# Performance work log

Measured on AMD Instinct MI355X. Metric: run time of the kernel, lower is better.

## Reference

```python
import jax, jax.numpy as jnp
import numpy as np

SIMPLE_W = 1.0
NON_SIMPLE_W = 5.0

# connectivity offset sets (exclude center)
_ALL26 = [(a, b, c) for a in (-1, 0, 1) for b in (-1, 0, 1) for c in (-1, 0, 1) if (a, b, c) != (0, 0, 0)]
OFF6 = [o for o in _ALL26 if abs(o[0]) + abs(o[1]) + abs(o[2]) == 1]          # scipy default structure
OFF18 = [o for o in _ALL26 if not (abs(o[0]) == 1 and abs(o[1]) == 1 and abs(o[2]) == 1)]  # the 's' structure
OFF26 = _ALL26                                                                  # np.ones((3,3,3))


def global_label(fg):
    """Connected-component labels (6-connectivity) via max-propagation.
    Labels are distinct positive ints per component (values differ from scipy's
    1..K but only label *equality* is used downstream). fg: bool [D,H,W]."""
    D, H, W = fg.shape
    idx = (jnp.arange(fg.size, dtype=jnp.int32) + 1).reshape(fg.shape)
    lab0 = jnp.where(fg, idx, 0)

    def step(lab):
        p = jnp.pad(lab, 1)
        m = lab
        for dz, dy, dx in OFF6:
            m = jnp.maximum(m, p[1 + dz:1 + dz + D, 1 + dy:1 + dy + H, 1 + dx:1 + dx + W])
        return jnp.where(fg, m, 0)

    def cond(c):
        return ~c[1]

    def body(c):
        lab, _ = c
        new = step(lab)
        return new, jnp.all(new == lab)

    lab, _ = jax.lax.while_loop(cond, body, (lab0, jnp.array(False)))
    return lab


def local_ncomp(mask, offsets):
    """Number of connected components inside each 3x3x3 window.
    mask: bool [N,3,3,3]. Max-propagation of unique seeds for 26 iters
    (>= max path length among 27 voxels); a component is counted where the
    surviving max label equals its own seed."""
    seed = (jnp.arange(27, dtype=jnp.int32) + 1).reshape(3, 3, 3)
    lab0 = jnp.where(mask, seed, 0)

    def body(_, lab):
        p = jnp.pad(lab, ((0, 0), (1, 1), (1, 1), (1, 1)))
        m = lab
        for dz, dy, dx in offsets:
            m = jnp.maximum(m, p[:, 1 + dz:4 + dz, 1 + dy:4 + dy, 1 + dx:4 + dx])
        return jnp.where(mask, m, 0)

    lab = jax.lax.fori_loop(0, 26, body, lab0)
    return jnp.sum((lab == seed) & mask, axis=(1, 2, 3))


def nonsimple_map(x):
    """Per-voxel non-simple-point indicator, float, same shape as x."""
    D, H, W = x.shape
    fg = x > 0
    glab = global_label(fg)
    p = jnp.pad(glab, 1, mode='edge')  # np.pad(..., 'edge')
    # 3x3x3 label windows per voxel -> [N,3,3,3]
    wins = jnp.stack([p[dz:dz + D, dy:dy + H, dx:dx + W]
                      for dz in range(3) for dy in range(3) for dx in range(3)], axis=-1)
    wins = wins.reshape(-1, 3, 3, 3)
    center = wins[:, 1, 1, 1]  # [N]
    c = center[:, None, None, None]
    # test 1: complement-of-center-label components (18-connectivity) must be exactly 1
    n1 = local_ncomp(wins != c, OFF18)
    # test 2: center-label components with center voxel removed (26-conn) must be exactly 1
    mask2 = (wins == c).at[:, 1, 1, 1].set(False)
    n2 = local_ncomp(mask2, OFF26)
    ns = (center != 0) & ((n1 != 1) | (n2 != 1))
    return ns.reshape(D, H, W).astype(x.dtype)


def setup_inputs() -> dict:
    key = jax.random.key(0)
    k1, k2 = jax.random.split(key)
    D = H = W = 64
    prediction = jax.random.normal(k1, (D, H, W), dtype=jnp.float32)
    label = jax.random.randint(k2, (D, H, W), 0, 2).astype(jnp.float32)
    return {"prediction": prediction, "label": label}


def reference(prediction, label):
    pw = nonsimple_map(prediction)
    lw = nonsimple_map(label)
    w_bool = (pw + lw) > 0
    weight = jnp.where(w_bool, NON_SIMPLE_W, SIMPLE_W).astype(prediction.dtype)
    # BCEWithLogitsLoss(reduction='none'): max(x,0) - x*y + log(1+exp(-|x|))
    cost = jnp.maximum(prediction, 0.0) - prediction * label + jnp.log1p(jnp.exp(-jnp.abs(prediction)))
    return jnp.mean(weight * cost)
```

## Files before the change

### kernel.cpp

```cpp
#include <hip/hip_runtime.h>

#define DIM 64
#define NVOX (DIM * DIM * DIM)
#define EPF 53248

__device__ __forceinline__ int find_root_link(int* L, int v) {
    for (;;) {
        int p = L[v];
        if (p == v) return v;
        int gp = L[p];
        if (gp == p) return p;
        L[v] = gp;
        v = gp;
    }
}

__device__ __forceinline__ void unite(int* L, int a, int b) {
    int ra = find_root_link(L, a);
    int rb = find_root_link(L, b);
    while (ra != rb) {
        if (ra > rb) { int t = ra; ra = rb; rb = t; }
        int old = atomicCAS(&L[rb], rb, ra);
        if (old == rb) break;
        rb = find_root_link(L, old);
        ra = find_root_link(L, ra);
    }
}

__device__ __forceinline__ int chase(const int* __restrict__ L, int p) {
    int q = L[p];
    while (q != p) { p = q; q = L[p]; }
    return p;
}

__global__ void local_ccl(const float* __restrict__ pred,
                          const float* __restrict__ lab,
                          int* __restrict__ LP, int* __restrict__ LL,
                          float* __restrict__ out) {
    __shared__ int s_lab[2048];
    int t = threadIdx.x;
    if (blockIdx.x == 0 && blockIdx.y == 0 && t == 0) *out = 0.0f;
    int b = blockIdx.x;
    int tx = b & 3, ty = (b >> 2) & 3, tz = b >> 4;
    int X0 = tx << 4, Y0 = ty << 4, Z0 = tz << 3;

    const float* src = blockIdx.y ? lab : pred;
    int* Lg = blockIdx.y ? LL : LP;

    bool fg[8];
    int vv[8];
#pragma unroll
    for (int i = 0; i < 8; ++i) {
        int l = t + (i << 8);
        int v = ((Z0 + (l >> 8)) << 12) | ((Y0 + ((l >> 4) & 15)) << 6)
              | (X0 + (l & 15));
        vv[i] = v;
        fg[i] = src[v] > 0.0f;
        s_lab[l] = fg[i] ? l : -1;
    }
    __syncthreads();

#pragma unroll
    for (int i = 0; i < 8; ++i) {
        if (!fg[i]) continue;
        int l = t + (i << 8);
        int lx = l & 15, ly = (l >> 4) & 15, lz = l >> 8;
        if (lx < 15 && s_lab[l + 1]   >= 0) unite(s_lab, l, l + 1);
        if (ly < 15 && s_lab[l + 16]  >= 0) unite(s_lab, l, l + 16);
        if (lz < 7  && s_lab[l + 256] >= 0) unite(s_lab, l, l + 256);
    }
    __syncthreads();

#pragma unroll
    for (int i = 0; i < 8; ++i) {
        int g = -1;
        if (fg[i]) {
            int p = s_lab[t + (i << 8)];
            while (s_lab[p] != p) p = s_lab[p];
            g = ((Z0 + (p >> 8)) << 12) | ((Y0 + ((p >> 4) & 15)) << 6)
              | (X0 + (p & 15));
        }
        Lg[vv[i]] = g;
    }
}

__global__ void boundary_link(int* __restrict__ LP, int* __restrict__ LL) {
    int r = blockIdx.x * blockDim.x + threadIdx.x;
    int v, n;
    if (r < 12288) {
        int plane = 15 + ((r >> 12) << 4);
        int ij = r & 4095;
        v = ((ij >> 6) << 12) | ((ij & 63) << 6) | plane;
        n = v + 1;
    } else if (r < 24576) {
        int r2 = r - 12288;
        int plane = 15 + ((r2 >> 12) << 4);
        int ij = r2 & 4095;
        v = ((ij >> 6) << 12) | (plane << 6) | (ij & 63);
        n = v + 64;
    } else {
        int r3 = r - 24576;
        int plane = 7 + ((r3 >> 12) << 3);
        int ij = r3 & 4095;
        v = (plane << 12) | ((ij >> 6) << 6) | (ij & 63);
        n = v + 4096;
    }

    int pa = LP[v], pb = LP[n];
    int la = LL[v], lb = LL[n];
    bool doP = (pa >= 0) & (pb >= 0);
    bool doL = (la >= 0) & (lb >= 0);

    int rp0 = -1, rp1 = -1, rl0 = -1, rl1 = -1;
    if (doP) {
        int x0 = chase(LP, pa), x1 = chase(LP, pb);
        rp0 = min(x0, x1); rp1 = max(x0, x1);
    }
    if (doL) {
        int x0 = chase(LL, la), x1 = chase(LL, lb);
        rl0 = min(x0, x1); rl1 = max(x0, x1);
    }

    int lane = threadIdx.x & 63;
    int qp0 = __shfl_up(rp0, 1, 64), qp1 = __shfl_up(rp1, 1, 64);
    int ql0 = __shfl_up(rl0, 1, 64), ql1 = __shfl_up(rl1, 1, 64);
    bool dupP = lane && (qp0 == rp0) && (qp1 == rp1);
    bool dupL = lane && (ql0 == rl0) && (ql1 == rl1);

    if (doP && !dupP && rp0 != rp1) unite(LP, rp0, rp1);
    if (doL && !dupL && rl0 != rl1) unite(LL, rl0, rl1);
}

#define MX_L 0x6DB6DB6u
#define MX_R 0x36DB6DBu
#define MY_L 0x7E3F1F8u
#define MY_R 0x0FC7E3Fu
#define M27  0x7FFFFFFu

__device__ __forceinline__ unsigned dil26(unsigned m) {
    m |= ((m << 1) & MX_L) | ((m >> 1) & MX_R);
    m |= ((m << 3) & MY_L) | ((m >> 3) & MY_R);
    m |= ((m << 9) & M27)  | (m >> 9);
    return m;
}
__device__ __forceinline__ unsigned dil18(unsigned m) {
    unsigned ax = m | ((m << 1) & MX_L) | ((m >> 1) & MX_R);
    unsigned ay = m | ((m << 3) & MY_L) | ((m >> 3) & MY_R);
    unsigned dxy = ax | ((ax << 3) & MY_L) | ((ax >> 3) & MY_R);
    unsigned dxz = ax | ((ax << 9) & M27)  | (ax >> 9);
    unsigned dyz = ay | ((ay << 9) & M27)  | (ay >> 9);
    return dxy | dxz | dyz;
}

__device__ __forceinline__ bool single18(unsigned m) {
    if (!m) return false;
    unsigned c = m & (~m + 1u);
    for (;;) {
        unsigned n = dil18(c) & m;
        if (n == m) return true;
        if (n == c) return false;
        c = n;
    }
}
__device__ __forceinline__ bool single26(unsigned m) {
    if (!m) return false;
    unsigned c = m & (~m + 1u);
    for (;;) {
        unsigned n = dil26(c) & m;
        if (n == m) return true;
        if (n == c) return false;
        c = n;
    }
}

#define HV 600

__global__ void finalize_kernel(const float* __restrict__ pred,
                                const float* __restrict__ lab,
                                const int* __restrict__ LP,
                                const int* __restrict__ LL,
                                float* __restrict__ out) {
    __shared__ int sP[HV], sL[HV];
    __shared__ float s_part[4];
    int t = threadIdx.x;
    int b = blockIdx.x;
    int tx = b & 7, ty = (b >> 3) & 7, tz = b >> 6;
    int x0 = tx << 3, y0 = ty << 3, z0 = tz << 2;

    for (int i = t; i < HV; i += 256) {
        int hx = i % 10, r = i / 10, hy = r % 10, hz = r / 10;
        int gx = x0 + hx - 1; gx = gx < 0 ? 0 : (gx > 63 ? 63 : gx);
        int gy = y0 + hy - 1; gy = gy < 0 ? 0 : (gy > 63 ? 63 : gy);
        int gz = z0 + hz - 1; gz = gz < 0 ? 0 : (gz > 63 ? 63 : gz);
        int gv = (gz << 12) | (gy << 6) | gx;
        int p = LP[gv];
        if (p >= 0) p = chase(LP, p);
        sP[i] = p;
        p = LL[gv];
        if (p >= 0) p = chase(LL, p);
        sL[i] = p;
    }
    __syncthreads();

    int lx = t & 7, ly = (t >> 3) & 7, lz = t >> 6;
    int x = x0 | lx, y = y0 | ly, z = z0 | lz;
    int v = (z << 12) | (y << 6) | x;
    int base = lz * 100 + ly * 10 + lx;

    bool nsP = false, nsL = false;
    {
        int c = sP[base + 111];
        if (c >= 0) {
            unsigned m1 = 0, m2 = 0; int k = 0;
#pragma unroll
            for (int kz = 0; kz < 3; ++kz)
#pragma unroll
                for (int ky = 0; ky < 3; ++ky)
#pragma unroll
                    for (int kx = 0; kx < 3; ++kx, ++k) {
                        int w = sP[base + kz * 100 + ky * 10 + kx];
                        m1 |= (unsigned)(w != c) << k;
                        m2 |= (unsigned)(w == c) << k;
                    }
            m2 &= ~(1u << 13);
            nsP = !(single18(m1) && single26(m2));
        }
    }
    {
        int c = sL[base + 111];
        if (c >= 0) {
            unsigned m1 = 0, m2 = 0; int k = 0;
#pragma unroll
            for (int kz = 0; kz < 3; ++kz)
#pragma unroll
                for (int ky = 0; ky < 3; ++ky)
#pragma unroll
                    for (int kx = 0; kx < 3; ++kx, ++k) {
                        int w = sL[base + kz * 100 + ky * 10 + kx];
                        m1 |= (unsigned)(w != c) << k;
                        m2 |= (unsigned)(w == c) << k;
                    }
            m2 &= ~(1u << 13);
            nsL = !(single18(m1) && single26(m2));
        }
    }

    float p = pred[v], l = lab[v];
    float cost = fmaxf(p, 0.0f) - p * l + log1pf(__expf(-fabsf(p)));
    float w = (nsP || nsL) ? 5.0f : 1.0f;
    float contrib = w * cost;

#pragma unroll
    for (int off = 32; off > 0; off >>= 1)
        contrib += __shfl_down(contrib, off, 64);
    if ((t & 63) == 0) s_part[t >> 6] = contrib;
    __syncthreads();
    if (t == 0) {
        float s = s_part[0] + s_part[1] + s_part[2] + s_part[3];
        atomicAdd(out, s * (1.0f / (float)NVOX));
    }
}

extern "C" void kernel_launch(void* const* d_in, const int* in_sizes, int n_in,
                              void* d_out, int out_size, void* d_ws, size_t ws_size,
                              hipStream_t stream) {
    const float* pred = (const float*)d_in[0];
    const float* lab  = (const float*)d_in[1];
    float* out = (float*)d_out;

    int* LP = (int*)d_ws;
    int* LL = LP + NVOX;

    hipLaunchKernelGGL(local_ccl, dim3(128, 2), dim3(256), 0, stream,
                       pred, lab, LP, LL, out);
    hipLaunchKernelGGL(boundary_link, dim3(EPF / 256), dim3(256), 0, stream,
                       LP, LL);
    hipLaunchKernelGGL(finalize_kernel, dim3(NVOX / 256), dim3(256), 0, stream,
                       pred, lab, LP, LL, out);
}
```

Baseline: 114.1 us.

## Enlarge finalize tiles to 8x8x8, batch halo loads, skip duplicate boundary chases

```diff
diff --git a/kernel.cpp b/kernel.cpp
--- a/kernel.cpp
+++ b/kernel.cpp
@@ -106,29 +106,35 @@
         n = v + 4096;
     }
 
+    int lane = threadIdx.x & 63;
+
     int pa = LP[v], pb = LP[n];
     int la = LL[v], lb = LL[n];
     bool doP = (pa >= 0) & (pb >= 0);
     bool doL = (la >= 0) & (lb >= 0);
 
+    int xpa = __shfl_up(pa, 1, 64), xpb = __shfl_up(pb, 1, 64);
+    int xla = __shfl_up(la, 1, 64), xlb = __shfl_up(lb, 1, 64);
+    if (lane && xpa == pa && xpb == pb) doP = false;
+    if (lane && xla == la && xlb == lb) doL = false;
+
     int rp0 = -1, rp1 = -1, rl0 = -1, rl1 = -1;
     if (doP) {
-        int x0 = chase(LP, pa), x1 = chase(LP, pb);
-        rp0 = min(x0, x1); rp1 = max(x0, x1);
+        int u0 = chase(LP, pa), u1 = chase(LP, pb);
+        rp0 = min(u0, u1); rp1 = max(u0, u1);
     }
     if (doL) {
-        int x0 = chase(LL, la), x1 = chase(LL, lb);
-        rl0 = min(x0, x1); rl1 = max(x0, x1);
-    }
-
-    int lane = threadIdx.x & 63;
+        int u0 = chase(LL, la), u1 = chase(LL, lb);
+        rl0 = min(u0, u1); rl1 = max(u0, u1);
+    }
+
     int qp0 = __shfl_up(rp0, 1, 64), qp1 = __shfl_up(rp1, 1, 64);
     int ql0 = __shfl_up(rl0, 1, 64), ql1 = __shfl_up(rl1, 1, 64);
     bool dupP = lane && (qp0 == rp0) && (qp1 == rp1);
     bool dupL = lane && (ql0 == rl0) && (ql1 == rl1);
 
-    if (doP && !dupP && rp0 != rp1) unite(LP, rp0, rp1);
-    if (doL && !dupL && rl0 != rl1) unite(LL, rl0, rl1);
+    if (rp0 >= 0 && rp0 != rp1 && !dupP) unite(LP, rp0, rp1);
+    if (rl0 >= 0 && rl0 != rl1 && !dupL) unite(LL, rl0, rl1);
 }
 
 #define MX_L 0x6DB6DB6u
@@ -173,7 +179,7 @@
     }
 }
 
-#define HV 600
+#define HV 1000
 
 __global__ void finalize_kernel(const float* __restrict__ pred,
                                 const float* __restrict__ lab,
@@ -184,76 +190,93 @@
     __shared__ float s_part[4];
     int t = threadIdx.x;
     int b = blockIdx.x;
-    int tx = b & 7, ty = (b >> 3) & 7, tz = b >> 6;
-    int x0 = tx << 3, y0 = ty << 3, z0 = tz << 2;
-
-    for (int i = t; i < HV; i += 256) {
-        int hx = i % 10, r = i / 10, hy = r % 10, hz = r / 10;
-        int gx = x0 + hx - 1; gx = gx < 0 ? 0 : (gx > 63 ? 63 : gx);
-        int gy = y0 + hy - 1; gy = gy < 0 ? 0 : (gy > 63 ? 63 : gy);
-        int gz = z0 + hz - 1; gz = gz < 0 ? 0 : (gz > 63 ? 63 : gz);
-        int gv = (gz << 12) | (gy << 6) | gx;
-        int p = LP[gv];
-        if (p >= 0) p = chase(LP, p);
-        sP[i] = p;
-        p = LL[gv];
-        if (p >= 0) p = chase(LL, p);
-        sL[i] = p;
+    int rx = b & 7, ry = (b >> 3) & 7, rz = b >> 6;
+    int x0 = rx << 3, y0 = ry << 3, z0 = rz << 3;
+
+    int pv[4], lv[4];
+#pragma unroll
+    for (int j = 0; j < 4; ++j) {
+        int i = t + (j << 8);
+        if (i < HV) {
+            int hx = i % 10, rr = i / 10, hy = rr % 10, hz = rr / 10;
+            int gx = x0 + hx - 1; gx = gx < 0 ? 0 : (gx > 63 ? 63 : gx);
+            int gy = y0 + hy - 1; gy = gy < 0 ? 0 : (gy > 63 ? 63 : gy);
+            int gz = z0 + hz - 1; gz = gz < 0 ? 0 : (gz > 63 ? 63 : gz);
+            int gv = (gz << 12) | (gy << 6) | gx;
+            pv[j] = LP[gv];
+            lv[j] = LL[gv];
+        }
+    }
+#pragma unroll
+    for (int j = 0; j < 4; ++j) {
+        int i = t + (j << 8);
+        if (i < HV) {
+            int p = pv[j];
+            if (p >= 0) p = chase(LP, p);
+            sP[i] = p;
+            p = lv[j];
+            if (p >= 0) p = chase(LL, p);
+            sL[i] = p;
+        }
     }
     __syncthreads();
 
-    int lx = t & 7, ly = (t >> 3) & 7, lz = t >> 6;
-    int x = x0 | lx, y = y0 | ly, z = z0 | lz;
-    int v = (z << 12) | (y << 6) | x;
-    int base = lz * 100 + ly * 10 + lx;
-
-    bool nsP = false, nsL = false;
-    {
-        int c = sP[base + 111];
-        if (c >= 0) {
-            unsigned m1 = 0, m2 = 0; int k = 0;
-#pragma unroll
-            for (int kz = 0; kz < 3; ++kz)
-#pragma unroll
-                for (int ky = 0; ky < 3; ++ky)
-#pragma unroll
-                    for (int kx = 0; kx < 3; ++kx, ++k) {
-                        int w = sP[base + kz * 100 + ky * 10 + kx];
-                        m1 |= (unsigned)(w != c) << k;
-                        m2 |= (unsigned)(w == c) << k;
-                    }
-            m2 &= ~(1u << 13);
-            nsP = !(single18(m1) && single26(m2));
-        }
-    }
-    {
-        int c = sL[base + 111];
-        if (c >= 0) {
-            unsigned m1 = 0, m2 = 0; int k = 0;
-#pragma unroll
-            for (int kz = 0; kz < 3; ++kz)
-#pragma unroll
-                for (int ky = 0; ky < 3; ++ky)
-#pragma unroll
-                    for (int kx = 0; kx < 3; ++kx, ++k) {
-                        int w = sL[base + kz * 100 + ky * 10 + kx];
-                        m1 |= (unsigned)(w != c) << k;
-                        m2 |= (unsigned)(w == c) << k;
-                    }
-            m2 &= ~(1u << 13);
-            nsL = !(single18(m1) && single26(m2));
-        }
-    }
-
-    float p = pred[v], l = lab[v];
-    float cost = fmaxf(p, 0.0f) - p * l + log1pf(__expf(-fabsf(p)));
-    float w = (nsP || nsL) ? 5.0f : 1.0f;
-    float contrib = w * cost;
+    float acc = 0.0f;
+#pragma unroll
+    for (int j = 0; j < 2; ++j) {
+        int l = t + (j << 8);
+        int lx = l & 7, ly = (l >> 3) & 7, lz = l >> 6;
+        int x = x0 | lx, y = y0 | ly, z = z0 | lz;
+        int v = (z << 12) | (y << 6) | x;
+        int base = lz * 100 + ly * 10 + lx;
+
+        bool nsP = false, nsL = false;
+        {
+            int c = sP[base + 111];
+            if (c >= 0) {
+                unsigned m1 = 0, m2 = 0; int k = 0;
+#pragma unroll
+                for (int kz = 0; kz < 3; ++kz)
+#pragma unroll
+                    for (int ky = 0; ky < 3; ++ky)
+#pragma unroll
+                        for (int kx = 0; kx < 3; ++kx, ++k) {
+                            int w = sP[base + kz * 100 + ky * 10 + kx];
+                            m1 |= (unsigned)(w != c) << k;
+                            m2 |= (unsigned)(w == c) << k;
+                        }
+                m2 &= ~(1u << 13);
+                nsP = !(single18(m1) && single26(m2));
+            }
+        }
+        {
+            int c = sL[base + 111];
+            if (c >= 0) {
+                unsigned m1 = 0, m2 = 0; int k = 0;
+#pragma unroll
+                for (int kz = 0; kz < 3; ++kz)
+#pragma unroll
+                    for (int ky = 0; ky < 3; ++ky)
+#pragma unroll
+                        for (int kx = 0; kx < 3; ++kx, ++k) {
+                            int w = sL[base + kz * 100 + ky * 10 + kx];
+                            m1 |= (unsigned)(w != c) << k;
+                            m2 |= (unsigned)(w == c) << k;
+                        }
+                m2 &= ~(1u << 13);
+                nsL = !(single18(m1) && single26(m2));
+            }
+        }
+
+        float p = pred[v], lvf = lab[v];
+        float cost = fmaxf(p, 0.0f) - p * lvf + log1pf(__expf(-fabsf(p)));
+        acc += ((nsP || nsL) ? 5.0f : 1.0f) * cost;
+    }
 
 #pragma unroll
     for (int off = 32; off > 0; off >>= 1)
-        contrib += __shfl_down(contrib, off, 64);
-    if ((t & 63) == 0) s_part[t >> 6] = contrib;
+        acc += __shfl_down(acc, off, 64);
+    if ((t & 63) == 0) s_part[t >> 6] = acc;
     __syncthreads();
     if (t == 0) {
         float s = s_part[0] + s_part[1] + s_part[2] + s_part[3];
@@ -275,6 +298,6 @@
                        pred, lab, LP, LL, out);
     hipLaunchKernelGGL(boundary_link, dim3(EPF / 256), dim3(256), 0, stream,
                        LP, LL);
-    hipLaunchKernelGGL(finalize_kernel, dim3(NVOX / 256), dim3(256), 0, stream,
+    hipLaunchKernelGGL(finalize_kernel, dim3(512), dim3(256), 0, stream,
                        pred, lab, LP, LL, out);
 }
```

Result: faster. 109.8 us (-3.7%).
